# Kernel tuning notes

Measured on AMD Instinct MI355X. Metric: run time of the kernel, lower is better.

The kernel has to match this reference:

```python
import jax, jax.numpy as jnp
import numpy as np

DIM = 512

def _ln(x, g, b, eps=1e-5):
    mu = jnp.mean(x, axis=-1, keepdims=True)
    var = jnp.mean(jnp.square(x - mu), axis=-1, keepdims=True)
    return (x - mu) * jax.lax.rsqrt(var + eps) * g + b

def setup_inputs() -> dict:
    key = jax.random.key(0)
    ks = jax.random.split(key, 12)
    B, S, D = 2, 4096, DIM
    w = lambda k: jax.random.normal(k, (D, D), jnp.float32) * (D ** -0.5)
    return {
        "text": jax.random.normal(ks[0], (B, S, D), jnp.float32),
        "img": jax.random.normal(ks[1], (B, S, D), jnp.float32),
        "ln_t_g": jnp.ones((D,), jnp.float32), "ln_t_b": jnp.zeros((D,), jnp.float32),
        "ln_i_g": jnp.ones((D,), jnp.float32), "ln_i_b": jnp.zeros((D,), jnp.float32),
        "Wq": w(ks[2]), "bq": jnp.zeros((D,), jnp.float32),
        "Wkt": w(ks[3]), "bkt": jnp.zeros((D,), jnp.float32),
        "Wvt": w(ks[4]), "bvt": jnp.zeros((D,), jnp.float32),
        "Wki": w(ks[5]), "bki": jnp.zeros((D,), jnp.float32),
        "Wvi": w(ks[6]), "bvi": jnp.zeros((D,), jnp.float32),
        "Wo": w(ks[7]), "bo": jnp.zeros((D,), jnp.float32),
    }

def reference(text, img, ln_t_g, ln_t_b, ln_i_g, ln_i_b,
              Wq, bq, Wkt, bkt, Wvt, bvt, Wki, bki, Wvi, bvi, Wo, bo):
    scale = DIM ** -0.5
    tn = _ln(text, ln_t_g, ln_t_b)   # [B,S,D]
    im = _ln(img, ln_i_g, ln_i_b)    # [B,S,D]
    norms = jnp.concatenate([tn, im], axis=0)          # [2B,S,D]
    K = jnp.concatenate([tn @ Wkt.T + bkt, im @ Wki.T + bki], axis=0)  # [2B,S,D]
    V = jnp.concatenate([tn @ Wvt.T + bvt, im @ Wvi.T + bvi], axis=0)  # [2B,S,D]
    q = norms @ Wq.T + bq                              # [2B,S,D]
    scores = jnp.einsum('bqd,bkd->bqk', q, K) * scale  # [2B,S,S]
    attn = jax.nn.softmax(scores, axis=-1)
    x = jnp.einsum('bqk,bkd->bqd', attn, V)            # [2B,S,D]
    x = x @ Wo.T + bo
    out = jnp.concatenate([_ln(x, ln_t_g, ln_t_b), _ln(x, ln_i_g, ln_i_b)], axis=0)  # [4B,S,D]
    return out
```

## Files before the change

### kernel.cpp

```cpp
#include <hip/hip_runtime.h>
#include <stdint.h>

#define SEQ 4096
#define DIM_ 512

typedef float f32x4 __attribute__((ext_vector_type(4)));
typedef short bf16x8 __attribute__((ext_vector_type(8)));

static __device__ __forceinline__ short f2bf(float f) {
  uint32_t u = __builtin_bit_cast(uint32_t, f);
  u += 0x7fffu + ((u >> 16) & 1u);
  return (short)(u >> 16);
}
static __device__ __forceinline__ float bf2f(short s) {
  uint32_t u = ((uint32_t)(uint16_t)s) << 16;
  return __builtin_bit_cast(float, u);
}
static __device__ __forceinline__ f32x4 zero4() {
  f32x4 z; z[0] = 0.f; z[1] = 0.f; z[2] = 0.f; z[3] = 0.f; return z;
}

static __device__ __forceinline__ void async_load16(const short* g, short* l) {
  __builtin_amdgcn_global_load_lds(
      (const __attribute__((address_space(1))) void*)g,
      (__attribute__((address_space(3))) void*)l,
      16, 0, 0);
}

__global__ __launch_bounds__(256) void ln_kernel(
    const float* __restrict__ text, const float* __restrict__ img,
    const float* __restrict__ gt, const float* __restrict__ bt,
    const float* __restrict__ gi, const float* __restrict__ bi,
    short* __restrict__ norms)
{
  int row = blockIdx.x;
  int batch = row >> 12;
  int tid = threadIdx.x;
  const float* g = (batch < 2) ? gt : gi;
  const float* b = (batch < 2) ? bt : bi;
  const float* src = (batch < 2) ? (text + (size_t)row * DIM_)
                                 : (img + (size_t)(row - 2 * SEQ) * DIM_);
  float x0 = src[tid], x1 = src[tid + 256];
  float s1 = x0 + x1, s2 = x0 * x0 + x1 * x1;
  #pragma unroll
  for (int off = 32; off; off >>= 1) { s1 += __shfl_xor(s1, off); s2 += __shfl_xor(s2, off); }
  __shared__ float rs1[4], rs2[4];
  int w = tid >> 6;
  if ((tid & 63) == 0) { rs1[w] = s1; rs2[w] = s2; }
  __syncthreads();
  float t1 = rs1[0] + rs1[1] + rs1[2] + rs1[3];
  float t2 = rs2[0] + rs2[1] + rs2[2] + rs2[3];
  float mu = t1 * (1.0f / DIM_);
  float var = t2 * (1.0f / DIM_) - mu * mu;
  float r = rsqrtf(var + 1e-5f);
  norms[(size_t)row * DIM_ + tid]       = f2bf((x0 - mu) * r * g[tid] + b[tid]);
  norms[(size_t)row * DIM_ + tid + 256] = f2bf((x1 - mu) * r * g[tid + 256] + b[tid + 256]);
}

__global__ __launch_bounds__(256) void prep_w(
    const float* __restrict__ Wq,  const float* __restrict__ Wkt, const float* __restrict__ Wvt,
    const float* __restrict__ Wki, const float* __restrict__ Wvi, const float* __restrict__ Wo,
    const float* __restrict__ bq,  const float* __restrict__ bkt, const float* __restrict__ bvt,
    const float* __restrict__ bki, const float* __restrict__ bvi,
    short* __restrict__ Wstack, short* __restrict__ WoB, float* __restrict__ bstack)
{
  int idx = blockIdx.x * 256 + threadIdx.x;
  const int WS = 4 * 1536 * 512;
  if (idx < WS) {
    int b = idx / 786432;
    int rem = idx - b * 786432;
    int rr = rem >> 9, cc = rem & 511;
    float v;
    if (rr < 512)       v = Wq[rr * 512 + cc];
    else if (rr < 1024) v = (b < 2 ? Wkt : Wki)[(rr - 512) * 512 + cc];
    else                v = (b < 2 ? Wvt : Wvi)[(rr - 1024) * 512 + cc];
    Wstack[idx] = f2bf(v);
  } else {
    int j = idx - WS;
    WoB[j] = f2bf(Wo[j]);
  }
  if (idx < 6144) {
    int b = idx / 1536, rr = idx - b * 1536;
    float v;
    if (rr < 512)       v = bq[rr];
    else if (rr < 1024) v = (b < 2 ? bkt : bki)[rr - 512];
    else                v = (b < 2 ? bvt : bvi)[rr - 1024];
    bstack[idx] = v;
  }
}

__global__ __launch_bounds__(256) void gemm_kernel(
    const short* __restrict__ A, long long aBS,
    const short* __restrict__ W, long long wBS,
    const float* __restrict__ bias, int bBS,
    short* __restrict__ out, long long outBS, long long segStride)
{
  __shared__ short As[128 * 72], Bs[128 * 72];
  int b = blockIdx.z;
  A += (size_t)b * aBS; W += (size_t)b * wBS; bias += (size_t)b * bBS;
  int m0 = blockIdx.x * 128, n0 = blockIdx.y * 128;
  int tid = threadIdx.x;
  int w = tid >> 6, lane = tid & 63, quad = lane >> 4, l16 = lane & 15;
  int wr = (w & 1) * 64, wc = (w >> 1) * 64;
  f32x4 acc[4][4];
  #pragma unroll
  for (int i = 0; i < 4; i++)
    #pragma unroll
    for (int j = 0; j < 4; j++) acc[i][j] = zero4();

  for (int kc = 0; kc < 8; ++kc) {
    __syncthreads();
    #pragma unroll
    for (int i = 0; i < 4; ++i) {
      int flat = i * 256 + tid;
      int r = flat >> 3, c = flat & 7;
      *(uint4*)(&As[r * 72 + c * 8]) = *(const uint4*)(A + (size_t)(m0 + r) * 512 + kc * 64 + c * 8);
      *(uint4*)(&Bs[r * 72 + c * 8]) = *(const uint4*)(W + (size_t)(n0 + r) * 512 + kc * 64 + c * 8);
    }
    __syncthreads();
    #pragma unroll
    for (int ks = 0; ks < 2; ++ks) {
      bf16x8 af[4], bfv[4];
      #pragma unroll
      for (int mi = 0; mi < 4; mi++)
        af[mi] = *(const bf16x8*)(&As[(wr + mi * 16 + l16) * 72 + ks * 32 + quad * 8]);
      #pragma unroll
      for (int ni = 0; ni < 4; ni++)
        bfv[ni] = *(const bf16x8*)(&Bs[(wc + ni * 16 + l16) * 72 + ks * 32 + quad * 8]);
      #pragma unroll
      for (int mi = 0; mi < 4; mi++)
        #pragma unroll
        for (int ni = 0; ni < 4; ni++)
          acc[mi][ni] = __builtin_amdgcn_mfma_f32_16x16x32_bf16(af[mi], bfv[ni], acc[mi][ni], 0, 0, 0);
    }
  }
  #pragma unroll
  for (int mi = 0; mi < 4; mi++) {
    #pragma unroll
    for (int ni = 0; ni < 4; ni++) {
      int ng = n0 + wc + ni * 16 + l16;
      int seg = ng >> 9, col = ng & 511;
      float bv = bias[ng];
      #pragma unroll
      for (int r = 0; r < 4; r++) {
        int mg = m0 + wr + mi * 16 + quad * 4 + r;
        out[(size_t)b * outBS + (size_t)seg * segStride + (size_t)mg * 512 + col] =
            f2bf(acc[mi][ni][r] + bv);
      }
    }
  }
}

__global__ __launch_bounds__(256) void transpose_kernel(const short* __restrict__ V, short* __restrict__ Vt)
{
  __shared__ short T[64 * 72];
  int b = blockIdx.z;
  int s0 = blockIdx.x * 64, d0 = blockIdx.y * 64;
  int tid = threadIdx.x;
  const short* Vb = V + (size_t)b * SEQ * 512;
  short* Vtb = Vt + (size_t)b * 512 * SEQ;
  #pragma unroll
  for (int i = 0; i < 2; ++i) {
    int flat = i * 256 + tid;
    int r = flat >> 3, c8 = flat & 7;
    bf16x8 v = *(const bf16x8*)(Vb + (size_t)(s0 + r) * 512 + d0 + c8 * 8);
    #pragma unroll
    for (int j = 0; j < 8; ++j) T[(c8 * 8 + j) * 72 + r] = v[j];
  }
  __syncthreads();
  #pragma unroll
  for (int i = 0; i < 2; ++i) {
    int flat = i * 256 + tid;
    int dl = flat & 63, sc = flat >> 6;
    uint4 v = *(const uint4*)(&T[dl * 72 + sc * 8]);
    *(uint4*)(Vtb + (size_t)(d0 + dl) * SEQ + s0 + sc * 8) = v;
  }
}

__global__ __launch_bounds__(256, 1) void attn_kernel(
    const short* __restrict__ Q, const short* __restrict__ K,
    const short* __restrict__ Vt, short* __restrict__ X)
{
  __shared__ short Ks[64 * 512];
  __shared__ short Vs[512 * 64];
  __shared__ short P[64 * 72];
  __shared__ float redm[2][64], reds[2][64], mst[64], lst[64], alph[64];

  int b = blockIdx.x >> 6, qt = blockIdx.x & 63;
  const short* Qb  = Q  + ((size_t)b * SEQ + qt * 64) * 512;
  const short* Kb  = K  + (size_t)b * SEQ * 512;
  const short* Vtb = Vt + (size_t)b * 512 * SEQ;
  short* Xb = X + ((size_t)b * SEQ + qt * 64) * 512;
  int tid = threadIdx.x;
  int w = tid >> 6, lane = tid & 63, quad = lane >> 4, l16 = lane & 15;
  int rg = w >> 1, kg = w & 1;
  const float cf = 0.044194173824159216f * 1.4426950408889634f;

  bf16x8 qf[2][16];
  #pragma unroll
  for (int mi = 0; mi < 2; mi++)
    #pragma unroll
    for (int ks = 0; ks < 16; ks++)
      qf[mi][ks] = *(const bf16x8*)(Qb + (size_t)(rg * 32 + mi * 16 + l16) * 512 + ks * 32 + quad * 8);

  if (tid < 64) { mst[tid] = -1e30f; lst[tid] = 0.f; }
  f32x4 o[4][8];
  #pragma unroll
  for (int i = 0; i < 4; i++)
    #pragma unroll
    for (int j = 0; j < 8; j++) o[i][j] = zero4();

  #pragma unroll
  for (int j = 0; j < 16; ++j) {
    int r = w * 16 + j;
    async_load16(Kb + (size_t)r * 512 + ((lane ^ (r & 15)) << 3), &Ks[r * 512]);
  }

  for (int kt = 0; kt < 64; ++kt) {
    __syncthreads();
    #pragma unroll
    for (int j = 0; j < 16; ++j) {
      int g = w * 16 + j;
      int row = g * 8 + (lane >> 3);
      int lc = (lane & 7) ^ (row & 7);
      async_load16(Vtb + (size_t)row * SEQ + kt * 64 + (lc << 3), &Vs[g * 8 * 64]);
    }

    f32x4 sacc[2][2];
    #pragma unroll
    for (int mi = 0; mi < 2; mi++)
      #pragma unroll
      for (int ni = 0; ni < 2; ni++) sacc[mi][ni] = zero4();
    #pragma unroll
    for (int ks = 0; ks < 16; ++ks) {
      bf16x8 bfv[2];
      #pragma unroll
      for (int ni = 0; ni < 2; ni++) {
        int row = kg * 32 + ni * 16 + l16;
        bfv[ni] = *(const bf16x8*)(&Ks[row * 512 + (((ks * 4 + quad) ^ l16) << 3)]);
      }
      #pragma unroll
      for (int mi = 0; mi < 2; mi++)
        #pragma unroll
        for (int ni = 0; ni < 2; ni++)
          sacc[mi][ni] = __builtin_amdgcn_mfma_f32_16x16x32_bf16(qf[mi][ks], bfv[ni], sacc[mi][ni], 0, 0, 0);
    }

    float lm[2][4];
    #pragma unroll
    for (int mi = 0; mi < 2; mi++)
      #pragma unroll
      for (int r = 0; r < 4; r++)
        lm[mi][r] = fmaxf(sacc[mi][0][r], sacc[mi][1][r]) * cf;
    #pragma unroll
    for (int off = 1; off <= 8; off <<= 1)
      #pragma unroll
      for (int mi = 0; mi < 2; mi++)
        #pragma unroll
        for (int r = 0; r < 4; r++) lm[mi][r] = fmaxf(lm[mi][r], __shfl_xor(lm[mi][r], off));
    if (l16 == 0) {
      #pragma unroll
      for (int mi = 0; mi < 2; mi++)
        #pragma unroll
        for (int r = 0; r < 4; r++)
          redm[kg][rg * 32 + mi * 16 + quad * 4 + r] = lm[mi][r];
    }
    __syncthreads();
    if (tid < 64) {
      float mt = fmaxf(redm[0][tid], redm[1][tid]);
      float mo = mst[tid];
      float mn = fmaxf(mo, mt);
      alph[tid] = exp2f(mo - mn);
      mst[tid] = mn;
    }
    __syncthreads();
    if (kt < 63) {
      #pragma unroll
      for (int j = 0; j < 16; ++j) {
        int r = w * 16 + j;
        async_load16(Kb + ((size_t)(kt + 1) * 64 + r) * 512 + ((lane ^ (r & 15)) << 3), &Ks[r * 512]);
      }
    }

    float ls[2][4];
    #pragma unroll
    for (int mi = 0; mi < 2; mi++)
      #pragma unroll
      for (int r = 0; r < 4; r++) ls[mi][r] = 0.f;
    #pragma unroll
    for (int mi = 0; mi < 2; mi++) {
      float mrow[4];
      #pragma unroll
      for (int r = 0; r < 4; r++) mrow[r] = mst[rg * 32 + mi * 16 + quad * 4 + r];
      #pragma unroll
      for (int ni = 0; ni < 2; ni++) {
        #pragma unroll
        for (int r = 0; r < 4; r++) {
          float p = exp2f(sacc[mi][ni][r] * cf - mrow[r]);
          ls[mi][r] += p;
          P[(rg * 32 + mi * 16 + quad * 4 + r) * 72 + kg * 32 + ni * 16 + l16] = f2bf(p);
        }
      }
    }
    #pragma unroll
    for (int off = 1; off <= 8; off <<= 1)
      #pragma unroll
      for (int mi = 0; mi < 2; mi++)
        #pragma unroll
        for (int r = 0; r < 4; r++) ls[mi][r] += __shfl_xor(ls[mi][r], off);
    if (l16 == 0) {
      #pragma unroll
      for (int mi = 0; mi < 2; mi++)
        #pragma unroll
        for (int r = 0; r < 4; r++)
          reds[kg][rg * 32 + mi * 16 + quad * 4 + r] = ls[mi][r];
    }
    #pragma unroll
    for (int om = 0; om < 4; om++) {
      float av[4];
      #pragma unroll
      for (int r = 0; r < 4; r++) av[r] = alph[om * 16 + quad * 4 + r];
      #pragma unroll
      for (int od = 0; od < 8; od++)
        #pragma unroll
        for (int r = 0; r < 4; r++) o[om][od][r] *= av[r];
    }
    __syncthreads();
    if (tid < 64) lst[tid] = alph[tid] * lst[tid] + reds[0][tid] + reds[1][tid];

    #pragma unroll
    for (int vc = 0; vc < 2; ++vc) {
      bf16x8 pa[4];
      #pragma unroll
      for (int om = 0; om < 4; om++)
        pa[om] = *(const bf16x8*)(&P[(om * 16 + l16) * 72 + vc * 32 + quad * 8]);
      #pragma unroll
      for (int od = 0; od < 8; od++) {
        int row = w * 128 + od * 16 + l16;
        bf16x8 vb = *(const bf16x8*)(&Vs[row * 64 + ((((vc * 4 + quad) ^ (l16 & 7))) << 3)]);
        #pragma unroll
        for (int om = 0; om < 4; om++)
          o[om][od] = __builtin_amdgcn_mfma_f32_16x16x32_bf16(pa[om], vb, o[om][od], 0, 0, 0);
      }
    }
  }
  __syncthreads();

  #pragma unroll
  for (int om = 0; om < 4; om++) {
    float li[4];
    #pragma unroll
    for (int r = 0; r < 4; r++) li[r] = 1.0f / lst[om * 16 + quad * 4 + r];
    #pragma unroll
    for (int od = 0; od < 8; od++)
      #pragma unroll
      for (int r = 0; r < 4; r++)
        Xb[(size_t)(om * 16 + quad * 4 + r) * 512 + w * 128 + od * 16 + l16] =
            f2bf(o[om][od][r] * li[r]);
  }
}

__global__ __launch_bounds__(256) void fln_kernel(
    const short* __restrict__ X2,
    const float* __restrict__ gt, const float* __restrict__ bt,
    const float* __restrict__ gi, const float* __restrict__ bi,
    float* __restrict__ out)
{
  int row = blockIdx.x;
  int tid = threadIdx.x;
  const short* src = X2 + (size_t)row * 512;
  float x0 = bf2f(src[tid]), x1 = bf2f(src[tid + 256]);
  float s1 = x0 + x1, s2 = x0 * x0 + x1 * x1;
  #pragma unroll
  for (int off = 32; off; off >>= 1) { s1 += __shfl_xor(s1, off); s2 += __shfl_xor(s2, off); }
  __shared__ float rs1[4], rs2[4];
  int w = tid >> 6;
  if ((tid & 63) == 0) { rs1[w] = s1; rs2[w] = s2; }
  __syncthreads();
  float t1 = rs1[0] + rs1[1] + rs1[2] + rs1[3];
  float t2 = rs2[0] + rs2[1] + rs2[2] + rs2[3];
  float mu = t1 * (1.0f / DIM_);
  float var = t2 * (1.0f / DIM_) - mu * mu;
  float r = rsqrtf(var + 1e-5f);
  float n0 = (x0 - mu) * r, n1 = (x1 - mu) * r;
  out[(size_t)row * 512 + tid]                   = n0 * gt[tid] + bt[tid];
  out[(size_t)row * 512 + tid + 256]             = n1 * gt[tid + 256] + bt[tid + 256];
  out[(size_t)(row + 16384) * 512 + tid]         = n0 * gi[tid] + bi[tid];
  out[(size_t)(row + 16384) * 512 + tid + 256]   = n1 * gi[tid + 256] + bi[tid + 256];
}

extern "C" void kernel_launch(void* const* d_in, const int* in_sizes, int n_in,
                              void* d_out, int out_size, void* d_ws, size_t ws_size,
                              hipStream_t stream) {
  const float* text  = (const float*)d_in[0];
  const float* img   = (const float*)d_in[1];
  const float* ln_t_g = (const float*)d_in[2];
  const float* ln_t_b = (const float*)d_in[3];
  const float* ln_i_g = (const float*)d_in[4];
  const float* ln_i_b = (const float*)d_in[5];
  const float* Wq  = (const float*)d_in[6];  const float* bq  = (const float*)d_in[7];
  const float* Wkt = (const float*)d_in[8];  const float* bkt = (const float*)d_in[9];
  const float* Wvt = (const float*)d_in[10]; const float* bvt = (const float*)d_in[11];
  const float* Wki = (const float*)d_in[12]; const float* bki = (const float*)d_in[13];
  const float* Wvi = (const float*)d_in[14]; const float* bvi = (const float*)d_in[15];
  const float* Wo  = (const float*)d_in[16]; const float* bo  = (const float*)d_in[17];

  const size_t NE = (size_t)4 * SEQ * DIM_;
  short* norms  = (short*)d_ws;
  short* Qp     = norms + NE;
  short* Kp     = Qp + NE;
  short* Vp     = Kp + NE;
  short* Vtp    = Vp + NE;
  short* Xp     = Vtp + NE;
  short* X2p    = Xp + NE;
  short* Wstack = X2p + NE;
  short* WoB    = Wstack + (size_t)4 * 1536 * 512;
  float* bstack = (float*)(WoB + (size_t)512 * 512);

  ln_kernel<<<dim3(16384), dim3(256), 0, stream>>>(text, img, ln_t_g, ln_t_b, ln_i_g, ln_i_b, norms);
  prep_w<<<dim3(13312), dim3(256), 0, stream>>>(Wq, Wkt, Wvt, Wki, Wvi, Wo,
                                                bq, bkt, bvt, bki, bvi, Wstack, WoB, bstack);
  gemm_kernel<<<dim3(32, 12, 4), dim3(256), 0, stream>>>(
      norms, (long long)(SEQ * DIM_), Wstack, (long long)(1536 * 512), bstack, 1536,
      Qp, (long long)(SEQ * DIM_), (long long)NE);
  transpose_kernel<<<dim3(64, 8, 4), dim3(256), 0, stream>>>(Vp, Vtp);
  attn_kernel<<<dim3(256), dim3(256), 0, stream>>>(Qp, Kp, Vtp, Xp);
  gemm_kernel<<<dim3(128, 4, 1), dim3(256), 0, stream>>>(
      Xp, 0LL, WoB, 0LL, bo, 0,
      X2p, 0LL, 0LL);
  fln_kernel<<<dim3(16384), dim3(256), 0, stream>>>(X2p, ln_t_g, ln_t_b, ln_i_g, ln_i_b, (float*)d_out);
}
```

Baseline: 667.2 us.

## Double attention block to 512 threads and split key and output columns across eight waves

The attention kernel now runs eight waves per block instead of four. The key dimension of each 64-key tile is split four ways, and the output head dimension is split eight ways. This halves per-wave MFMA work, cuts the output accumulators, and lets more waves per SIMD hide LDS and softmax-sync latency. In exchange, every wave still holds the full Q fragments, the reduction arrays grow to four partials, and more threads join each block-wide barrier.

```diff
diff --git a/kernel.cpp b/kernel.cpp
--- a/kernel.cpp
+++ b/kernel.cpp
@@ -177,14 +177,14 @@
   }
 }
 
-__global__ __launch_bounds__(256, 1) void attn_kernel(
+__global__ __launch_bounds__(512, 2) void attn_kernel(
     const short* __restrict__ Q, const short* __restrict__ K,
     const short* __restrict__ Vt, short* __restrict__ X)
 {
   __shared__ short Ks[64 * 512];
   __shared__ short Vs[512 * 64];
   __shared__ short P[64 * 72];
-  __shared__ float redm[2][64], reds[2][64], mst[64], lst[64], alph[64];
+  __shared__ float redm[4][64], reds[4][64], mst[64], lst[64], alph[64];
 
   int b = blockIdx.x >> 6, qt = blockIdx.x & 63;
   const short* Qb  = Q  + ((size_t)b * SEQ + qt * 64) * 512;
@@ -193,7 +193,7 @@
   short* Xb = X + ((size_t)b * SEQ + qt * 64) * 512;
   int tid = threadIdx.x;
   int w = tid >> 6, lane = tid & 63, quad = lane >> 4, l16 = lane & 15;
-  int rg = w >> 1, kg = w & 1;
+  int rg = w >> 2, kg = w & 3;
   const float cf = 0.044194173824159216f * 1.4426950408889634f;
 
   bf16x8 qf[2][16];
@@ -204,54 +204,44 @@
       qf[mi][ks] = *(const bf16x8*)(Qb + (size_t)(rg * 32 + mi * 16 + l16) * 512 + ks * 32 + quad * 8);
 
   if (tid < 64) { mst[tid] = -1e30f; lst[tid] = 0.f; }
-  f32x4 o[4][8];
+  f32x4 o[4][4];
   #pragma unroll
   for (int i = 0; i < 4; i++)
     #pragma unroll
-    for (int j = 0; j < 8; j++) o[i][j] = zero4();
-
-  #pragma unroll
-  for (int j = 0; j < 16; ++j) {
-    int r = w * 16 + j;
+    for (int j = 0; j < 4; j++) o[i][j] = zero4();
+
+  #pragma unroll
+  for (int j = 0; j < 8; ++j) {
+    int r = w * 8 + j;
     async_load16(Kb + (size_t)r * 512 + ((lane ^ (r & 15)) << 3), &Ks[r * 512]);
   }
 
   for (int kt = 0; kt < 64; ++kt) {
     __syncthreads();
     #pragma unroll
-    for (int j = 0; j < 16; ++j) {
-      int g = w * 16 + j;
+    for (int j = 0; j < 8; ++j) {
+      int g = w * 8 + j;
       int row = g * 8 + (lane >> 3);
       int lc = (lane & 7) ^ (row & 7);
       async_load16(Vtb + (size_t)row * SEQ + kt * 64 + (lc << 3), &Vs[g * 8 * 64]);
     }
 
-    f32x4 sacc[2][2];
+    f32x4 sacc[2];
+    sacc[0] = zero4(); sacc[1] = zero4();
+    #pragma unroll
+    for (int ks = 0; ks < 16; ++ks) {
+      int row = kg * 16 + l16;
+      bf16x8 bfv = *(const bf16x8*)(&Ks[row * 512 + (((ks * 4 + quad) ^ l16) << 3)]);
+      #pragma unroll
+      for (int mi = 0; mi < 2; mi++)
+        sacc[mi] = __builtin_amdgcn_mfma_f32_16x16x32_bf16(qf[mi][ks], bfv, sacc[mi], 0, 0, 0);
+    }
+
+    float lm[2][4];
     #pragma unroll
     for (int mi = 0; mi < 2; mi++)
       #pragma unroll
-      for (int ni = 0; ni < 2; ni++) sacc[mi][ni] = zero4();
-    #pragma unroll
-    for (int ks = 0; ks < 16; ++ks) {
-      bf16x8 bfv[2];
-      #pragma unroll
-      for (int ni = 0; ni < 2; ni++) {
-        int row = kg * 32 + ni * 16 + l16;
-        bfv[ni] = *(const bf16x8*)(&Ks[row * 512 + (((ks * 4 + quad) ^ l16) << 3)]);
-      }
-      #pragma unroll
-      for (int mi = 0; mi < 2; mi++)
-        #pragma unroll
-        for (int ni = 0; ni < 2; ni++)
-          sacc[mi][ni] = __builtin_amdgcn_mfma_f32_16x16x32_bf16(qf[mi][ks], bfv[ni], sacc[mi][ni], 0, 0, 0);
-    }
-
-    float lm[2][4];
-    #pragma unroll
-    for (int mi = 0; mi < 2; mi++)
-      #pragma unroll
-      for (int r = 0; r < 4; r++)
-        lm[mi][r] = fmaxf(sacc[mi][0][r], sacc[mi][1][r]) * cf;
+      for (int r = 0; r < 4; r++) lm[mi][r] = sacc[mi][r] * cf;
     #pragma unroll
     for (int off = 1; off <= 8; off <<= 1)
       #pragma unroll
@@ -267,7 +257,7 @@
     }
     __syncthreads();
     if (tid < 64) {
-      float mt = fmaxf(redm[0][tid], redm[1][tid]);
+      float mt = fmaxf(fmaxf(redm[0][tid], redm[1][tid]), fmaxf(redm[2][tid], redm[3][tid]));
       float mo = mst[tid];
       float mn = fmaxf(mo, mt);
       alph[tid] = exp2f(mo - mn);
@@ -276,30 +266,23 @@
     __syncthreads();
     if (kt < 63) {
       #pragma unroll
-      for (int j = 0; j < 16; ++j) {
-        int r = w * 16 + j;
+      for (int j = 0; j < 8; ++j) {
+        int r = w * 8 + j;
         async_load16(Kb + ((size_t)(kt + 1) * 64 + r) * 512 + ((lane ^ (r & 15)) << 3), &Ks[r * 512]);
       }
     }
 
     float ls[2][4];
     #pragma unroll
-    for (int mi = 0; mi < 2; mi++)
-      #pragma unroll
-      for (int r = 0; r < 4; r++) ls[mi][r] = 0.f;
-    #pragma unroll
     for (int mi = 0; mi < 2; mi++) {
       float mrow[4];
       #pragma unroll
       for (int r = 0; r < 4; r++) mrow[r] = mst[rg * 32 + mi * 16 + quad * 4 + r];
       #pragma unroll
-      for (int ni = 0; ni < 2; ni++) {
-        #pragma unroll
-        for (int r = 0; r < 4; r++) {
-          float p = exp2f(sacc[mi][ni][r] * cf - mrow[r]);
-          ls[mi][r] += p;
-          P[(rg * 32 + mi * 16 + quad * 4 + r) * 72 + kg * 32 + ni * 16 + l16] = f2bf(p);
-        }
+      for (int r = 0; r < 4; r++) {
+        float p = exp2f(sacc[mi][r] * cf - mrow[r]);
+        ls[mi][r] = p;
+        P[(rg * 32 + mi * 16 + quad * 4 + r) * 72 + kg * 16 + l16] = f2bf(p);
       }
     }
     #pragma unroll
@@ -321,12 +304,13 @@
       #pragma unroll
       for (int r = 0; r < 4; r++) av[r] = alph[om * 16 + quad * 4 + r];
       #pragma unroll
-      for (int od = 0; od < 8; od++)
+      for (int od = 0; od < 4; od++)
         #pragma unroll
         for (int r = 0; r < 4; r++) o[om][od][r] *= av[r];
     }
     __syncthreads();
-    if (tid < 64) lst[tid] = alph[tid] * lst[tid] + reds[0][tid] + reds[1][tid];
+    if (tid < 64)
+      lst[tid] = alph[tid] * lst[tid] + reds[0][tid] + reds[1][tid] + reds[2][tid] + reds[3][tid];
 
     #pragma unroll
     for (int vc = 0; vc < 2; ++vc) {
@@ -335,8 +319,8 @@
       for (int om = 0; om < 4; om++)
         pa[om] = *(const bf16x8*)(&P[(om * 16 + l16) * 72 + vc * 32 + quad * 8]);
       #pragma unroll
-      for (int od = 0; od < 8; od++) {
-        int row = w * 128 + od * 16 + l16;
+      for (int od = 0; od < 4; od++) {
+        int row = w * 64 + od * 16 + l16;
         bf16x8 vb = *(const bf16x8*)(&Vs[row * 64 + ((((vc * 4 + quad) ^ (l16 & 7))) << 3)]);
         #pragma unroll
         for (int om = 0; om < 4; om++)
@@ -352,10 +336,10 @@
     #pragma unroll
     for (int r = 0; r < 4; r++) li[r] = 1.0f / lst[om * 16 + quad * 4 + r];
     #pragma unroll
-    for (int od = 0; od < 8; od++)
+    for (int od = 0; od < 4; od++)
       #pragma unroll
       for (int r = 0; r < 4; r++)
-        Xb[(size_t)(om * 16 + quad * 4 + r) * 512 + w * 128 + od * 16 + l16] =
+        Xb[(size_t)(om * 16 + quad * 4 + r) * 512 + w * 64 + od * 16 + l16] =
             f2bf(o[om][od][r] * li[r]);
   }
 }
@@ -424,7 +408,7 @@
       norms, (long long)(SEQ * DIM_), Wstack, (long long)(1536 * 512), bstack, 1536,
       Qp, (long long)(SEQ * DIM_), (long long)NE);
   transpose_kernel<<<dim3(64, 8, 4), dim3(256), 0, stream>>>(Vp, Vtp);
-  attn_kernel<<<dim3(256), dim3(256), 0, stream>>>(Qp, Kp, Vtp, Xp);
+  attn_kernel<<<dim3(256), dim3(512), 0, stream>>>(Qp, Kp, Vtp, Xp);
   gemm_kernel<<<dim3(128, 4, 1), dim3(256), 0, stream>>>(
       Xp, 0LL, WoB, 0LL, bo, 0,
       X2p, 0LL, 0LL);
```

Result: slower. 816.7 us (+22.4%).
